# Performance work log

Measured on AMD Instinct MI355X. Metric: run time of the kernel, lower is better.

The kernel has to match this reference:

```python
import jax, jax.numpy as jnp
import numpy as np

N_SRC0, N_FTRS, N_HID, N_CLS = 200000, 128, 1500, 64
E0, E1 = 1600000, 500000
RES0, RES1 = 50000, 10000


def sage_conv(x, src, tgt, res_size, W_root, W_neigh, b):
    # mean aggregation of neighbor (source) features onto the first res_size target nodes
    msg = x[src]                                              # [E, F] gather
    summed = jax.ops.segment_sum(msg, tgt, num_segments=res_size)   # [res, F]
    cnt = jax.ops.segment_sum(jnp.ones((src.shape[0],), x.dtype), tgt, num_segments=res_size)
    mean = summed / jnp.maximum(cnt, 1.0)[:, None]
    return x[:res_size] @ W_root + mean @ W_neigh + b


def setup_inputs() -> dict:
    key = jax.random.key(0)
    ks = jax.random.split(key, 12)
    x = jax.random.normal(ks[0], (N_SRC0, N_FTRS), dtype=jnp.float32)
    edge_src0 = jax.random.randint(ks[1], (E0,), 0, N_SRC0)
    edge_tgt0 = jax.random.randint(ks[2], (E0,), 0, RES0)
    edge_src1 = jax.random.randint(ks[3], (E1,), 0, RES0)
    edge_tgt1 = jax.random.randint(ks[4], (E1,), 0, RES1)
    s1 = 1.0 / np.sqrt(N_FTRS)
    s2 = 1.0 / np.sqrt(N_HID)
    W1_root = jax.random.uniform(ks[5], (N_FTRS, N_HID), jnp.float32, -s1, s1)
    W1_neigh = jax.random.uniform(ks[6], (N_FTRS, N_HID), jnp.float32, -s1, s1)
    b1 = jax.random.uniform(ks[7], (N_HID,), jnp.float32, -s1, s1)
    W2_root = jax.random.uniform(ks[8], (N_HID, N_CLS), jnp.float32, -s2, s2)
    W2_neigh = jax.random.uniform(ks[9], (N_HID, N_CLS), jnp.float32, -s2, s2)
    b2 = jax.random.uniform(ks[10], (N_CLS,), jnp.float32, -s2, s2)
    return {
        "x": x,
        "W1_root": W1_root, "W1_neigh": W1_neigh, "b1": b1,
        "W2_root": W2_root, "W2_neigh": W2_neigh, "b2": b2,
        "edge_src0": edge_src0, "edge_tgt0": edge_tgt0,
        "edge_src1": edge_src1, "edge_tgt1": edge_tgt1,
        "res0": RES0, "res1": RES1,
    }


def reference(x, W1_root, W1_neigh, b1, W2_root, W2_neigh, b2,
              edge_src0, edge_tgt0, edge_src1, edge_tgt1, res0, res1):
    h = sage_conv(x, edge_src0, edge_tgt0, res0, W1_root, W1_neigh, b1)  # [res0, H]
    h = jax.nn.relu(h)
    # dropout p=0.5 is identity in eval mode
    out = sage_conv(h, edge_src1, edge_tgt1, res1, W2_root, W2_neigh, b2)  # [res1, C]
    return jax.nn.log_softmax(out, axis=1)
```

## Files before the change

### kernel.cpp

```cpp
#include <hip/hip_runtime.h>
#include <hip/hip_bf16.h>
#include <cstdint>
#include <cstddef>

#define NSRC   200000
#define NF     128
#define NHID   1500
#define NHIDP  1536
#define NCLS   64
#define E0N    1600000
#define E1N    500000
#define RES0   50000
#define RES1   10000

#define CH     4096
#define NCH0   ((E0N + CH - 1) / CH)
#define NCH1   ((E1N + CH - 1) / CH)
#define NB0    ((RES0 + 255) / 256)
#define NB1    ((RES1 + 255) / 256)

#define PREP_BLOCKS  ((256 * NHIDP + 128 * NHIDP + NHIDP + 255) / 256)
#define COPYX_BLOCKS ((NSRC * NF) / (256 * 8))

typedef __bf16 bf16x8 __attribute__((ext_vector_type(8)));
typedef float  f32x4  __attribute__((ext_vector_type(4)));
typedef unsigned short u16x8 __attribute__((ext_vector_type(8)));
typedef unsigned int u32;
typedef unsigned long long u64;

__device__ __forceinline__ unsigned short f2bf(float f) {
    union { float f; unsigned u; } v; v.f = f;
    unsigned r = v.u + 0x7fffu + ((v.u >> 16) & 1u);
    return (unsigned short)(r >> 16);
}
__device__ __forceinline__ float bf2f(unsigned short b) {
    union { u32 u; float f; } v; v.u = ((u32)b) << 16;
    return v.f;
}

__device__ __forceinline__ u32 cvt_pk_bf16(float lo, float hi) {
    u32 r;
    asm("v_cvt_pk_bf16_f32 %0, %1, %2" : "=v"(r) : "v"(lo), "v"(hi));
    return r;
}

__device__ __forceinline__ void lds_dma16(const void* g, void* lds) {
    __builtin_amdgcn_global_load_lds(
        (const __attribute__((address_space(1))) unsigned int*)g,
        (__attribute__((address_space(3))) unsigned int*)lds, 16, 0, 0);
}

__device__ __forceinline__ void raw_barrier() {
    __asm__ volatile("s_barrier" ::: "memory");
}
__device__ __forceinline__ void wait_vm4() {
    __asm__ volatile("s_waitcnt vmcnt(4)" ::: "memory");
}
__device__ __forceinline__ void wait_vm0() {
    __asm__ volatile("s_waitcnt vmcnt(0)" ::: "memory");
}

__global__ __launch_bounds__(256) void setup_kernel(
        const float* __restrict__ x, unsigned short* __restrict__ xbf,
        const float* __restrict__ W1r, const float* __restrict__ W1n,
        const float* __restrict__ b1,
        const float* __restrict__ W2r, const float* __restrict__ W2n,
        unsigned short* __restrict__ WcatT, unsigned short* __restrict__ W2f,
        float* __restrict__ b1e) {
    int bid = blockIdx.x;
    if (bid < PREP_BLOCKS) {
        int id = bid * 256 + threadIdx.x;
        if (id < 256 * NHIDP) {
            int n = id >> 8, k = id & 255;
            float v = 0.f;
            if (n < NHID) v = (k < NF) ? W1r[k * NHID + n] : W1n[(k - NF) * NHID + n];
            WcatT[n * 256 + k] = f2bf(v);
        } else {
            int id2 = id - 256 * NHIDP;
            if (id2 < 128 * NHIDP) {
                int n = id2 / NHIDP, k = id2 % NHIDP;
                float v = 0.f;
                if (k < NHID) v = (n < 64) ? W2n[k * 64 + n] : W2r[k * 64 + (n - 64)];
                int j = k >> 7, w = k & 127;
                int kk = w >> 5, r = w & 31;
                int hi = r >> 4, qd = (r >> 2) & 3, e = r & 3;
                W2f[(((size_t)(j * 4 + kk) * 128 + n) * 32) + qd * 8 + hi * 4 + e] = f2bf(v);
            } else {
                int c = id2 - 128 * NHIDP;
                if (c < NHIDP) b1e[c] = (c < NHID) ? b1[c] : 0.f;
            }
        }
    } else {
        size_t i = ((size_t)(bid - PREP_BLOCKS) * 256 + threadIdx.x) * 8;
        const float4* s = (const float4*)(x + i);
        float4 a = s[0], b = s[1];
        u16x8 o;
        o[0] = f2bf(a.x); o[1] = f2bf(a.y); o[2] = f2bf(a.z); o[3] = f2bf(a.w);
        o[4] = f2bf(b.x); o[5] = f2bf(b.y); o[6] = f2bf(b.z); o[7] = f2bf(b.w);
        *(u16x8*)(xbf + i) = o;
    }
}

__device__ __forceinline__ void p1a_body(const int* __restrict__ tgt, int n,
                                         int nb, u32* __restrict__ H, int c) {
    __shared__ u32 lhist[256];
    int tid = threadIdx.x;
    lhist[tid] = 0;
    __syncthreads();
#pragma unroll
    for (int it = 0; it < CH / 256; ++it) {
        int i = c * CH + it * 256 + tid;
        if (i < n) atomicAdd(&lhist[((u32)tgt[i]) >> 8], 1u);
    }
    __syncthreads();
    if (tid < nb) H[c * nb + tid] = lhist[tid];
}

__global__ __launch_bounds__(256) void p1a_both_kernel(
        const int* __restrict__ t0, const int* __restrict__ t1,
        u32* __restrict__ H1, u32* __restrict__ H2) {
    int b = blockIdx.x;
    if (b < NCH0) p1a_body(t0, E0N, NB0, H1, b);
    else          p1a_body(t1, E1N, NB1, H2, b - NCH0);
}

__device__ __forceinline__ void bscan_body(const u32* __restrict__ H,
                                           int nch, int nb, int b,
                                           u32* __restrict__ base_rel,
                                           u32* __restrict__ Bsum) {
    __shared__ u32 part[512];
    int t = threadIdx.x;
    part[t] = (t < nch) ? H[t * nb + b] : 0u;
    __syncthreads();
    for (int d = 1; d < 512; d <<= 1) {
        u32 v = part[t];
        u32 add = (t >= d) ? part[t - d] : 0u;
        __syncthreads();
        part[t] = v + add;
        __syncthreads();
    }
    if (t < nch) base_rel[t * nb + b] = (t == 0) ? 0u : part[t - 1];
    if (t == 0) Bsum[b] = part[nch - 1];
}

__global__ __launch_bounds__(512) void bscan_both_kernel(
        const u32* __restrict__ H1, u32* __restrict__ base1, u32* __restrict__ Bsum1,
        const u32* __restrict__ H2, u32* __restrict__ base2, u32* __restrict__ Bsum2) {
    int b = blockIdx.x;
    if (b < NB0) bscan_body(H1, NCH0, NB0, b, base1, Bsum1);
    else         bscan_body(H2, NCH1, NB1, b - NB0, base2, Bsum2);
}

__global__ __launch_bounds__(256) void boff_kernel(const u32* __restrict__ Bsum1,
                                                   u32* __restrict__ boff1, int nb1,
                                                   const u32* __restrict__ Bsum2,
                                                   u32* __restrict__ boff2, int nb2) {
    const u32* B = blockIdx.x ? Bsum2 : Bsum1;
    u32* O = blockIdx.x ? boff2 : boff1;
    int nb = blockIdx.x ? nb2 : nb1;
    __shared__ u32 part[256];
    int t = threadIdx.x;
    part[t] = (t < nb) ? B[t] : 0u;
    __syncthreads();
    for (int d = 1; d < 256; d <<= 1) {
        u32 v = part[t];
        u32 add = (t >= d) ? part[t - d] : 0u;
        __syncthreads();
        part[t] = v + add;
        __syncthreads();
    }
    if (t < nb) O[t] = (t == 0) ? 0u : part[t - 1];
}

__device__ __forceinline__ void p1b_body(const int* __restrict__ src,
                                         const int* __restrict__ tgt, int n,
                                         int nb, const u32* __restrict__ base_rel,
                                         const u32* __restrict__ boff,
                                         u64* __restrict__ bucketed, int c) {
    __shared__ u32 lcur[256];
    __shared__ u32 lbase[256];
    int tid = threadIdx.x;
    lcur[tid] = 0;
    if (tid < nb) lbase[tid] = base_rel[c * nb + tid] + boff[tid];
    __syncthreads();
#pragma unroll
    for (int it = 0; it < CH / 256; ++it) {
        int i = c * CH + it * 256 + tid;
        if (i < n) {
            u32 t = (u32)tgt[i];
            u32 s = (u32)src[i];
            u32 b = t >> 8;
            u32 r = atomicAdd(&lcur[b], 1u);
            bucketed[lbase[b] + r] = ((u64)t << 32) | (u64)s;
        }
    }
}

__global__ __launch_bounds__(256) void p1b_both_kernel(
        const int* __restrict__ s0, const int* __restrict__ t0,
        const u32* __restrict__ base1, const u32* __restrict__ boff1,
        u64* __restrict__ bkt1,
        const int* __restrict__ s1, const int* __restrict__ t1,
        const u32* __restrict__ base2, const u32* __restrict__ boff2,
        u64* __restrict__ bkt2) {
    int b = blockIdx.x;
    if (b < NCH0) p1b_body(s0, t0, E0N, NB0, base1, boff1, bkt1, b);
    else          p1b_body(s1, t1, E1N, NB1, base2, boff2, bkt2, b - NCH0);
}

__device__ __forceinline__ void p2_body(const u64* __restrict__ bucketed,
                                        const u32* __restrict__ boff,
                                        int nb, int res, int etot,
                                        int* __restrict__ csr,
                                        u32* __restrict__ off_out,
                                        u32* __restrict__ cnt_out, int b) {
    __shared__ u32 lhist[256];
    __shared__ u32 part[256];
    __shared__ u32 cur[256];
    int tid = threadIdx.x;
    u32 start = boff[b];
    u32 end = (b == nb - 1) ? (u32)etot : boff[b + 1];
    u32 count = end - start;
    if (tid < 256) lhist[tid] = 0;
    __syncthreads();
    for (u32 i = tid; i < count; i += 1024) {
        u32 t = (u32)(bucketed[start + i] >> 32);
        atomicAdd(&lhist[t & 255u], 1u);
    }
    __syncthreads();
    if (tid < 256) part[tid] = lhist[tid];
    __syncthreads();
    for (int d = 1; d < 256; d <<= 1) {
        u32 v = (tid < 256) ? part[tid] : 0u;
        u32 add = (tid >= d && tid < 256) ? part[tid - d] : 0u;
        __syncthreads();
        if (tid < 256) part[tid] = v + add;
        __syncthreads();
    }
    if (tid < 256) {
        u32 excl = (tid == 0) ? 0u : part[tid - 1];
        cur[tid] = excl;
        int tg = (b << 8) + tid;
        if (tg < res) {
            off_out[tg] = start + excl;
            cnt_out[tg] = lhist[tid];
        }
    }
    __syncthreads();
    for (u32 i = tid; i < count; i += 1024) {
        u64 pr = bucketed[start + i];
        u32 lt = ((u32)(pr >> 32)) & 255u;
        u32 r = atomicAdd(&cur[lt], 1u);
        csr[start + r] = (int)(u32)pr;
    }
}

__global__ __launch_bounds__(1024) void p2_both_kernel(
        const u64* __restrict__ bkt1, const u32* __restrict__ boff1,
        int* __restrict__ csr1, u32* __restrict__ off1, u32* __restrict__ cnt1,
        const u64* __restrict__ bkt2, const u32* __restrict__ boff2,
        int* __restrict__ csr2, u32* __restrict__ off2, u32* __restrict__ cnt2) {
    int b = blockIdx.x;
    if (b < NB0) p2_body(bkt1, boff1, NB0, RES0, E0N, csr1, off1, cnt1, b);
    else         p2_body(bkt2, boff2, NB1, RES1, E1N, csr2, off2, cnt2, b - NB0);
}

__global__ __launch_bounds__(256) void agg1_csr_kernel(
        const unsigned short* __restrict__ xbf, const int* __restrict__ csr,
        const u32* __restrict__ off, const u32* __restrict__ cnt,
        unsigned short* __restrict__ mean1) {
    int row = blockIdx.x * 4 + (threadIdx.x >> 6);
    int lane = threadIdx.x & 63;
    if (row >= RES0) return;
    int q = lane >> 4, c16 = lane & 15;
    u32 base = off[row], deg = cnt[row];
    float acc[8] = {};
    u32 e = 0;
    for (; e + 8 <= deg; e += 8) {
        int s0 = csr[base + e + q];
        int s1 = csr[base + e + 4 + q];
        u16x8 v0 = *(const u16x8*)(xbf + (size_t)s0 * NF + c16 * 8);
        u16x8 v1 = *(const u16x8*)(xbf + (size_t)s1 * NF + c16 * 8);
#pragma unroll
        for (int i = 0; i < 8; ++i) acc[i] += bf2f(v0[i]) + bf2f(v1[i]);
    }
    for (; e + 4 <= deg; e += 4) {
        int s0 = csr[base + e + q];
        u16x8 v0 = *(const u16x8*)(xbf + (size_t)s0 * NF + c16 * 8);
#pragma unroll
        for (int i = 0; i < 8; ++i) acc[i] += bf2f(v0[i]);
    }
    if (e < deg) {
        bool valid = (e + q) < deg;
        int s0 = csr[base + (valid ? e + q : e)];
        u16x8 v0 = *(const u16x8*)(xbf + (size_t)s0 * NF + c16 * 8);
        if (valid) {
#pragma unroll
            for (int i = 0; i < 8; ++i) acc[i] += bf2f(v0[i]);
        }
    }
#pragma unroll
    for (int i = 0; i < 8; ++i) {
        acc[i] += __shfl_xor(acc[i], 32, 64);
        acc[i] += __shfl_xor(acc[i], 16, 64);
    }
    if (q == 0) {
        float inv = 1.0f / fmaxf((float)deg, 1.0f);
        u16x8 o;
#pragma unroll
        for (int i = 0; i < 8; ++i) o[i] = f2bf(acc[i] * inv);
        *(u16x8*)(mean1 + (size_t)row * NF + c16 * 8) = o;
    }
}

__device__ __forceinline__ void stage_chunk(
        const unsigned short* __restrict__ xbf, const unsigned short* __restrict__ mean1,
        const unsigned short* __restrict__ WcatT, int m0, int j, int kt,
        unsigned short* As, unsigned short* Bs, int wid, int lane) {
    int ksel = kt * 32;
    const unsigned short* srcA = (ksel < 128)
        ? xbf + (size_t)m0 * NF + ksel
        : mean1 + (size_t)m0 * NF + (ksel - 128);
#pragma unroll
    for (int ci = 0; ci < 2; ++ci) {
        int cb = ci * 256 + wid * 64;
        int chunk = cb + lane;
        int n = chunk >> 2, kc = (chunk & 3) ^ (n & 3);
        lds_dma16(srcA + (size_t)n * NF + kc * 8, &As[cb * 8]);
    }
    const unsigned short* srcB = WcatT + (size_t)(j * 128) * 256 + ksel;
#pragma unroll
    for (int ci = 0; ci < 2; ++ci) {
        int cb = ci * 256 + wid * 64;
        int chunk = cb + lane;
        int n = chunk >> 2, kc = (chunk & 3) ^ (n & 3);
        lds_dma16(srcB + (size_t)n * 256 + kc * 8, &Bs[cb * 8]);
    }
}

__global__ __launch_bounds__(256, 2) void fused_gemm_kernel(
        const unsigned short* __restrict__ xbf, const unsigned short* __restrict__ mean1,
        const unsigned short* __restrict__ WcatT, const float* __restrict__ b1e,
        const unsigned short* __restrict__ W2f,
        unsigned short* __restrict__ pnbf, float* __restrict__ root64) {
    __shared__ __align__(16) unsigned short As[3][128 * 32];
    __shared__ __align__(16) unsigned short Bs[3][128 * 32];

    int m0 = blockIdx.x * 128;
    int tid = threadIdx.x;
    int lane = tid & 63, wid = tid >> 6;
    int wm = wid;
    int quad = lane >> 4, l15 = lane & 15;
    const int csw = (quad ^ (l15 & 3)) * 8;

    f32x4 pacc[2][8] = {};

    stage_chunk(xbf, mean1, WcatT, m0, 0, 0, As[0], Bs[0], wid, lane);
    stage_chunk(xbf, mean1, WcatT, m0, 0, 1, As[1], Bs[1], wid, lane);

#pragma unroll 1
    for (int jj = 0; jj < 12; ++jj) {
        const int j = jj;
        f32x4 hacc[2][8] = {};
#pragma unroll
        for (int kt = 0; kt < 8; ++kt) {
            const int g = jj * 8 + kt;
            if (g == 95) wait_vm0(); else wait_vm4();
            raw_barrier();
            if (g + 2 < 96) {
                int g2 = g + 2;
                stage_chunk(xbf, mean1, WcatT, m0, g2 >> 3, g2 & 7,
                            As[g2 % 3], Bs[g2 % 3], wid, lane);
            }
            const unsigned short* Asb = As[g % 3];
            const unsigned short* Bsb = Bs[g % 3];
            bf16x8 a[2], b[8];
#pragma unroll
            for (int mi = 0; mi < 2; ++mi)
                a[mi] = *(const bf16x8*)(&Asb[(wm * 32 + mi * 16 + l15) * 32 + csw]);
#pragma unroll
            for (int ni = 0; ni < 8; ++ni)
                b[ni] = *(const bf16x8*)(&Bsb[(ni * 16 + l15) * 32 + csw]);
            __builtin_amdgcn_s_setprio(1);
#pragma unroll
            for (int mi = 0; mi < 2; ++mi)
#pragma unroll
                for (int ni = 0; ni < 8; ++ni)
                    hacc[mi][ni] = __builtin_amdgcn_mfma_f32_16x16x32_bf16(b[ni], a[mi], hacc[mi][ni], 0, 0, 0);
            __builtin_amdgcn_s_setprio(0);
        }

        u32 a2w[2][4][4];
#pragma unroll
        for (int ni = 0; ni < 8; ++ni) {
            float4 bv = *(const float4*)(b1e + j * 128 + ni * 16 + quad * 4);
#pragma unroll
            for (int mi = 0; mi < 2; ++mi) {
                f32x4 h = hacc[mi][ni];
                float h0 = fmaxf(h[0] + bv.x, 0.f);
                float h1 = fmaxf(h[1] + bv.y, 0.f);
                float h2 = fmaxf(h[2] + bv.z, 0.f);
                float h3 = fmaxf(h[3] + bv.w, 0.f);
                a2w[mi][ni >> 1][(ni & 1) * 2 + 0] = cvt_pk_bf16(h0, h1);
                a2w[mi][ni >> 1][(ni & 1) * 2 + 1] = cvt_pk_bf16(h2, h3);
            }
        }
        __builtin_amdgcn_s_setprio(1);
#pragma unroll
        for (int kk = 0; kk < 4; ++kk) {
            union U { u32 w[4]; bf16x8 v; uint4 q; };
            U A2[2];
#pragma unroll
            for (int mi = 0; mi < 2; ++mi)
#pragma unroll
                for (int w = 0; w < 4; ++w) A2[mi].w[w] = a2w[mi][kk][w];
            const unsigned short* wp =
                W2f + ((size_t)(j * 4 + kk) * 128) * 32 + (size_t)quad * 8;
#pragma unroll
            for (int ni2 = 0; ni2 < 8; ++ni2) {
                U B2;
                B2.q = *(const uint4*)(wp + (size_t)(ni2 * 16 + l15) * 32);
#pragma unroll
                for (int mi = 0; mi < 2; ++mi)
                    pacc[mi][ni2] = __builtin_amdgcn_mfma_f32_16x16x32_bf16(B2.v, A2[mi].v, pacc[mi][ni2], 0, 0, 0);
            }
        }
        __builtin_amdgcn_s_setprio(0);
    }

#pragma unroll
    for (int mi = 0; mi < 2; ++mi) {
        int gr = m0 + wm * 32 + mi * 16 + l15;
        if (gr < RES0) {
#pragma unroll
            for (int ni2 = 0; ni2 < 8; ++ni2) {
                f32x4 s = pacc[mi][ni2];
                if (ni2 < 4) {
                    uint2 o;
                    o.x = (u32)f2bf(s[0]) | ((u32)f2bf(s[1]) << 16);
                    o.y = (u32)f2bf(s[2]) | ((u32)f2bf(s[3]) << 16);
                    *(uint2*)(pnbf + (size_t)gr * 64 + ni2 * 16 + quad * 4) = o;
                } else if (gr < RES1) {
                    *(f32x4*)(root64 + (size_t)gr * 64 + (ni2 - 4) * 16 + quad * 4) = s;
                }
            }
        }
    }
}

__global__ __launch_bounds__(256) void final_csr_kernel(
        const unsigned short* __restrict__ pnbf, const float* __restrict__ root64,
        const int* __restrict__ csr, const u32* __restrict__ off,
        const u32* __restrict__ cnt, const float* __restrict__ b2,
        float* __restrict__ out) {
    int row = blockIdx.x * 4 + (threadIdx.x >> 6);
    int lane = threadIdx.x & 63;
    if (row >= RES1) return;
    int es = lane >> 3, c8 = lane & 7;
    u32 base = off[row], deg = cnt[row];
    float acc[8] = {};
    u32 e = 0;
    for (; e + 8 <= deg; e += 8) {
        int s = csr[base + e + es];
        u16x8 v = *(const u16x8*)(pnbf + (size_t)s * 64 + c8 * 8);
#pragma unroll
        for (int i = 0; i < 8; ++i) acc[i] += bf2f(v[i]);
    }
    if (e < deg) {
        bool valid = (e + es) < deg;
        int s = csr[base + (valid ? e + es : e)];
        u16x8 v = *(const u16x8*)(pnbf + (size_t)s * 64 + c8 * 8);
        if (valid) {
#pragma unroll
            for (int i = 0; i < 8; ++i) acc[i] += bf2f(v[i]);
        }
    }
#pragma unroll
    for (int i = 0; i < 8; ++i) {
        acc[i] += __shfl_xor(acc[i], 32, 64);
        acc[i] += __shfl_xor(acc[i], 16, 64);
        acc[i] += __shfl_xor(acc[i], 8, 64);
    }
    float inv = 1.0f / fmaxf((float)deg, 1.0f);
    float v[8];
    const float* rp = root64 + (size_t)row * 64 + c8 * 8;
#pragma unroll
    for (int i = 0; i < 8; ++i) v[i] = rp[i] + acc[i] * inv + b2[c8 * 8 + i];
    float m = v[0];
#pragma unroll
    for (int i = 1; i < 8; ++i) m = fmaxf(m, v[i]);
    m = fmaxf(m, __shfl_xor(m, 1, 64));
    m = fmaxf(m, __shfl_xor(m, 2, 64));
    m = fmaxf(m, __shfl_xor(m, 4, 64));
    float s = 0.f;
#pragma unroll
    for (int i = 0; i < 8; ++i) s += expf(v[i] - m);
    s += __shfl_xor(s, 1, 64);
    s += __shfl_xor(s, 2, 64);
    s += __shfl_xor(s, 4, 64);
    if (es == 0) {
        float lg = logf(s);
        f32x4 o0, o1;
#pragma unroll
        for (int i = 0; i < 4; ++i) { o0[i] = v[i] - m - lg; o1[i] = v[i + 4] - m - lg; }
        *(f32x4*)(&out[(size_t)row * 64 + c8 * 8])     = o0;
        *(f32x4*)(&out[(size_t)row * 64 + c8 * 8 + 4]) = o1;
    }
}

extern "C" void kernel_launch(void* const* d_in, const int* in_sizes, int n_in,
                              void* d_out, int out_size, void* d_ws, size_t ws_size,
                              hipStream_t stream) {
    const float* x   = (const float*)d_in[0];
    const float* W1r = (const float*)d_in[1];
    const float* W1n = (const float*)d_in[2];
    const float* b1  = (const float*)d_in[3];
    const float* W2r = (const float*)d_in[4];
    const float* W2n = (const float*)d_in[5];
    const float* b2  = (const float*)d_in[6];
    const int* es0 = (const int*)d_in[7];
    const int* et0 = (const int*)d_in[8];
    const int* es1 = (const int*)d_in[9];
    const int* et1 = (const int*)d_in[10];
    float* out = (float*)d_out;

    char* ws = (char*)d_ws;
    size_t off_ = 0;
    auto alloc = [&](size_t bytes) {
        void* ptr = ws + off_;
        off_ = (off_ + bytes + 255) & ~(size_t)255;
        return ptr;
    };
    u64* bkt1  = (u64*)alloc((size_t)E0N * 8);
    u64* bkt2  = (u64*)alloc((size_t)E1N * 8);
    int* csr1  = (int*)alloc((size_t)E0N * 4);
    u32* H1    = (u32*)alloc((size_t)NCH0 * NB0 * 4);
    u32* base1 = (u32*)alloc((size_t)NCH0 * NB0 * 4);
    u32* H2    = (u32*)alloc((size_t)NCH1 * NB1 * 4);
    u32* base2 = (u32*)alloc((size_t)NCH1 * NB1 * 4);
    u32* Bsum1 = (u32*)alloc((size_t)NB0 * 4);
    u32* Bsum2 = (u32*)alloc((size_t)NB1 * 4);
    u32* boff1 = (u32*)alloc((size_t)NB0 * 4);
    u32* boff2 = (u32*)alloc((size_t)NB1 * 4);
    u32* off1  = (u32*)alloc((size_t)RES0 * 4);
    u32* cnt1  = (u32*)alloc((size_t)RES0 * 4);
    int* csr2  = (int*)alloc((size_t)E1N * 4);
    u32* off2  = (u32*)alloc((size_t)RES1 * 4);
    u32* cnt2  = (u32*)alloc((size_t)RES1 * 4);
    unsigned short* xbf    = (unsigned short*)alloc((size_t)NSRC * NF * 2);
    unsigned short* mean1  = (unsigned short*)alloc((size_t)(RES0 + 128) * NF * 2);
    unsigned short* WcatT  = (unsigned short*)alloc((size_t)NHIDP * 256 * 2);
    unsigned short* W2f    = (unsigned short*)alloc((size_t)128 * NHIDP * 2);
    float*          b1e    = (float*)alloc((size_t)NHIDP * 4);
    unsigned short* pnbf   = (unsigned short*)alloc((size_t)RES0 * 64 * 2);
    float*          root64 = (float*)alloc((size_t)RES1 * 64 * 4);

    setup_kernel<<<PREP_BLOCKS + COPYX_BLOCKS, 256, 0, stream>>>(
        x, xbf, W1r, W1n, b1, W2r, W2n, WcatT, W2f, b1e);

    p1a_both_kernel<<<NCH0 + NCH1, 256, 0, stream>>>(et0, et1, H1, H2);
    bscan_both_kernel<<<NB0 + NB1, 512, 0, stream>>>(H1, base1, Bsum1, H2, base2, Bsum2);
    boff_kernel<<<2, 256, 0, stream>>>(Bsum1, boff1, NB0, Bsum2, boff2, NB1);
    p1b_both_kernel<<<NCH0 + NCH1, 256, 0, stream>>>(
        es0, et0, base1, boff1, bkt1, es1, et1, base2, boff2, bkt2);
    p2_both_kernel<<<NB0 + NB1, 1024, 0, stream>>>(
        bkt1, boff1, csr1, off1, cnt1, bkt2, boff2, csr2, off2, cnt2);

    agg1_csr_kernel<<<(RES0 + 3) / 4, 256, 0, stream>>>(
        xbf, csr1, off1, cnt1, mean1);

    fused_gemm_kernel<<<(RES0 + 127) / 128, 256, 0, stream>>>(
        xbf, mean1, WcatT, b1e, W2f, pnbf, root64);

    final_csr_kernel<<<(RES1 + 3) / 4, 256, 0, stream>>>(
        pnbf, root64, csr2, off2, cnt2, b2, out);
}
```

Baseline: 438.5 us.

## Merge histogram into setup kernel, deepen GEMM pipeline, unroll gather by 16

Folds the edge-target histogram pass into the setup kernel as extra blocks, which removes one launch and lets the histogram run alongside the weight and feature conversion. The fused GEMM now uses four LDS stages with a prefetch distance of three instead of three stages and distance two, so more global loads are in flight. The CSR gather gains a 16-edge unrolled loop that exposes more independent loads per iteration. The larger LDS footprint (64 KB per block) may cut occupancy below the requested two blocks per CU, and the extra loads raise register pressure.

```diff
diff --git a/kernel.cpp b/kernel.cpp
--- a/kernel.cpp
+++ b/kernel.cpp
@@ -53,11 +53,29 @@
 __device__ __forceinline__ void raw_barrier() {
     __asm__ volatile("s_barrier" ::: "memory");
 }
+__device__ __forceinline__ void wait_vm8() {
+    __asm__ volatile("s_waitcnt vmcnt(8)" ::: "memory");
+}
 __device__ __forceinline__ void wait_vm4() {
     __asm__ volatile("s_waitcnt vmcnt(4)" ::: "memory");
 }
 __device__ __forceinline__ void wait_vm0() {
     __asm__ volatile("s_waitcnt vmcnt(0)" ::: "memory");
+}
+
+__device__ __forceinline__ void p1a_body(const int* __restrict__ tgt, int n,
+                                         int nb, u32* __restrict__ H, int c) {
+    __shared__ u32 lhist[256];
+    int tid = threadIdx.x;
+    lhist[tid] = 0;
+    __syncthreads();
+#pragma unroll
+    for (int it = 0; it < CH / 256; ++it) {
+        int i = c * CH + it * 256 + tid;
+        if (i < n) atomicAdd(&lhist[((u32)tgt[i]) >> 8], 1u);
+    }
+    __syncthreads();
+    if (tid < nb) H[c * nb + tid] = lhist[tid];
 }
 
 __global__ __launch_bounds__(256) void setup_kernel(
@@ -66,7 +84,9 @@
         const float* __restrict__ b1,
         const float* __restrict__ W2r, const float* __restrict__ W2n,
         unsigned short* __restrict__ WcatT, unsigned short* __restrict__ W2f,
-        float* __restrict__ b1e) {
+        float* __restrict__ b1e,
+        const int* __restrict__ t0, const int* __restrict__ t1,
+        u32* __restrict__ H1, u32* __restrict__ H2) {
     int bid = blockIdx.x;
     if (bid < PREP_BLOCKS) {
         int id = bid * 256 + threadIdx.x;
@@ -90,7 +110,7 @@
                 if (c < NHIDP) b1e[c] = (c < NHID) ? b1[c] : 0.f;
             }
         }
-    } else {
+    } else if (bid < PREP_BLOCKS + COPYX_BLOCKS) {
         size_t i = ((size_t)(bid - PREP_BLOCKS) * 256 + threadIdx.x) * 8;
         const float4* s = (const float4*)(x + i);
         float4 a = s[0], b = s[1];
@@ -98,30 +118,11 @@
         o[0] = f2bf(a.x); o[1] = f2bf(a.y); o[2] = f2bf(a.z); o[3] = f2bf(a.w);
         o[4] = f2bf(b.x); o[5] = f2bf(b.y); o[6] = f2bf(b.z); o[7] = f2bf(b.w);
         *(u16x8*)(xbf + i) = o;
-    }
-}
-
-__device__ __forceinline__ void p1a_body(const int* __restrict__ tgt, int n,
-                                         int nb, u32* __restrict__ H, int c) {
-    __shared__ u32 lhist[256];
-    int tid = threadIdx.x;
-    lhist[tid] = 0;
-    __syncthreads();
-#pragma unroll
-    for (int it = 0; it < CH / 256; ++it) {
-        int i = c * CH + it * 256 + tid;
-        if (i < n) atomicAdd(&lhist[((u32)tgt[i]) >> 8], 1u);
-    }
-    __syncthreads();
-    if (tid < nb) H[c * nb + tid] = lhist[tid];
-}
-
-__global__ __launch_bounds__(256) void p1a_both_kernel(
-        const int* __restrict__ t0, const int* __restrict__ t1,
-        u32* __restrict__ H1, u32* __restrict__ H2) {
-    int b = blockIdx.x;
-    if (b < NCH0) p1a_body(t0, E0N, NB0, H1, b);
-    else          p1a_body(t1, E1N, NB1, H2, b - NCH0);
+    } else {
+        int c = bid - (PREP_BLOCKS + COPYX_BLOCKS);
+        if (c < NCH0) p1a_body(t0, E0N, NB0, H1, c);
+        else          p1a_body(t1, E1N, NB1, H2, c - NCH0);
+    }
 }
 
 __device__ __forceinline__ void bscan_body(const u32* __restrict__ H,
@@ -276,6 +277,19 @@
     u32 base = off[row], deg = cnt[row];
     float acc[8] = {};
     u32 e = 0;
+    for (; e + 16 <= deg; e += 16) {
+        int s0 = csr[base + e + q];
+        int s1 = csr[base + e + 4 + q];
+        int s2 = csr[base + e + 8 + q];
+        int s3 = csr[base + e + 12 + q];
+        u16x8 v0 = *(const u16x8*)(xbf + (size_t)s0 * NF + c16 * 8);
+        u16x8 v1 = *(const u16x8*)(xbf + (size_t)s1 * NF + c16 * 8);
+        u16x8 v2 = *(const u16x8*)(xbf + (size_t)s2 * NF + c16 * 8);
+        u16x8 v3 = *(const u16x8*)(xbf + (size_t)s3 * NF + c16 * 8);
+#pragma unroll
+        for (int i = 0; i < 8; ++i)
+            acc[i] += (bf2f(v0[i]) + bf2f(v1[i])) + (bf2f(v2[i]) + bf2f(v3[i]));
+    }
     for (; e + 8 <= deg; e += 8) {
         int s0 = csr[base + e + q];
         int s1 = csr[base + e + 4 + q];
@@ -343,8 +357,8 @@
         const unsigned short* __restrict__ WcatT, const float* __restrict__ b1e,
         const unsigned short* __restrict__ W2f,
         unsigned short* __restrict__ pnbf, float* __restrict__ root64) {
-    __shared__ __align__(16) unsigned short As[3][128 * 32];
-    __shared__ __align__(16) unsigned short Bs[3][128 * 32];
+    __shared__ __align__(16) unsigned short As[4][128 * 32];
+    __shared__ __align__(16) unsigned short Bs[4][128 * 32];
 
     int m0 = blockIdx.x * 128;
     int tid = threadIdx.x;
@@ -357,6 +371,7 @@
 
     stage_chunk(xbf, mean1, WcatT, m0, 0, 0, As[0], Bs[0], wid, lane);
     stage_chunk(xbf, mean1, WcatT, m0, 0, 1, As[1], Bs[1], wid, lane);
+    stage_chunk(xbf, mean1, WcatT, m0, 0, 2, As[2], Bs[2], wid, lane);
 
 #pragma unroll 1
     for (int jj = 0; jj < 12; ++jj) {
@@ -365,15 +380,17 @@
 #pragma unroll
         for (int kt = 0; kt < 8; ++kt) {
             const int g = jj * 8 + kt;
-            if (g == 95) wait_vm0(); else wait_vm4();
+            if (g <= 93) wait_vm8();
+            else if (g == 94) wait_vm4();
+            else wait_vm0();
             raw_barrier();
-            if (g + 2 < 96) {
-                int g2 = g + 2;
-                stage_chunk(xbf, mean1, WcatT, m0, g2 >> 3, g2 & 7,
-                            As[g2 % 3], Bs[g2 % 3], wid, lane);
+            if (g + 3 < 96) {
+                int g3 = g + 3;
+                stage_chunk(xbf, mean1, WcatT, m0, g3 >> 3, g3 & 7,
+                            As[g3 & 3], Bs[g3 & 3], wid, lane);
             }
-            const unsigned short* Asb = As[g % 3];
-            const unsigned short* Bsb = Bs[g % 3];
+            const unsigned short* Asb = As[g & 3];
+            const unsigned short* Bsb = Bs[g & 3];
             bf16x8 a[2], b[8];
 #pragma unroll
             for (int mi = 0; mi < 2; ++mi)
@@ -555,10 +572,9 @@
     unsigned short* pnbf   = (unsigned short*)alloc((size_t)RES0 * 64 * 2);
     float*          root64 = (float*)alloc((size_t)RES1 * 64 * 4);
 
-    setup_kernel<<<PREP_BLOCKS + COPYX_BLOCKS, 256, 0, stream>>>(
-        x, xbf, W1r, W1n, b1, W2r, W2n, WcatT, W2f, b1e);
-
-    p1a_both_kernel<<<NCH0 + NCH1, 256, 0, stream>>>(et0, et1, H1, H2);
+    setup_kernel<<<PREP_BLOCKS + COPYX_BLOCKS + NCH0 + NCH1, 256, 0, stream>>>(
+        x, xbf, W1r, W1n, b1, W2r, W2n, WcatT, W2f, b1e, et0, et1, H1, H2);
+
     bscan_both_kernel<<<NB0 + NB1, 512, 0, stream>>>(H1, base1, Bsum1, H2, base2, Bsum2);
     boff_kernel<<<2, 256, 0, stream>>>(Bsum1, boff1, NB0, Bsum2, boff2, NB1);
     p1b_both_kernel<<<NCH0 + NCH1, 256, 0, stream>>>(
```

New measurement: 434.6 us. No clear change (-0.9%).
